# Kernel tuning notes

Measured on AMD Instinct MI355X. Metric: run time of the kernel, lower is better.

## Reference

```python
import jax, jax.numpy as jnp
import numpy as np

N, C, T, H, W = 8, 512, 8, 32, 32
CI = 256          # inter_channels = in_channels // 2
CA = 128          # audio feature dim (hard-coded nn.Linear(128, in_channels))
BN_EPS = 1e-5
LN_EPS = 1e-5


def setup_inputs() -> dict:
    key = jax.random.key(0)
    ks = jax.random.split(key, 8)
    s = 0.02
    f32 = jnp.float32
    return {
        "x": jax.random.normal(ks[0], (N, C, T, H, W), f32),
        "audio": jax.random.normal(ks[1], (N, T, CA), f32),
        "align_W": jax.random.normal(ks[2], (C, CA), f32) * s,
        "align_b": jnp.zeros((C,), f32),
        "Wg": jax.random.normal(ks[3], (CI, C), f32) * s,
        "bg": jnp.zeros((CI,), f32),
        "Wth": jax.random.normal(ks[4], (CI, C), f32) * s,
        "bth": jnp.zeros((CI,), f32),
        "Wph": jax.random.normal(ks[5], (CI, C), f32) * s,
        "bph": jnp.zeros((CI,), f32),
        "Wz": jax.random.normal(ks[6], (C, CI), f32) * s,
        "bz": jnp.zeros((C,), f32),
        "bn_gamma": jnp.ones((C,), f32),
        "bn_beta": jnp.zeros((C,), f32),
        "ln_gamma": jnp.ones((C,), f32),
        "ln_beta": jnp.zeros((C,), f32),
    }


def reference(x, audio, align_W, align_b, Wg, bg, Wth, bth, Wph, bph,
              Wz, bz, bn_gamma, bn_beta, ln_gamma, ln_beta):
    n, c, t, h, w = x.shape
    thw = t * h * w

    # align_channel: Linear(128, C) + ReLU on audio (N,T,128) -> (N,T,C)
    audio_temp = jax.nn.relu(jnp.einsum('ntk,ck->ntc', audio, align_W) + align_b)
    a = audio_temp.transpose(0, 2, 1)  # (N,C,T); broadcast over (H,W) kept implicit

    # 1x1x1 conv projections (== per-token linear maps)
    g_x = (jnp.einsum('oc,ncthw->nthwo', Wg, x) + bg).reshape(n, thw, CI)      # (N,THW,CI)
    theta_x = (jnp.einsum('oc,ncthw->nthwo', Wth, x) + bth).reshape(n, thw, CI)
    phi_a = jnp.einsum('oc,nct->not', Wph, a) + bph[None, :, None]             # (N,CI,T)

    # mode='dot' attention. phi(audio) is constant over (h,w): the full score
    # matrix f[n,s,(t,h,w)] equals f_small[n,s,t], so f@g factorizes exactly.
    f_small = jnp.einsum('nsi,nit->nst', theta_x, phi_a)   # (N,THW,T)
    f_div = f_small / thw                                  # f / N_tokens
    G = g_x.reshape(n, t, h * w, CI).sum(axis=2)           # (N,T,CI): sum of g over repeated hw
    y = jnp.einsum('nst,nto->nso', f_div, G)               # (N,THW,CI)
    y = y.transpose(0, 2, 1).reshape(n, CI, t, h, w)

    # W_z: 1x1x1 conv (CI->C) + BatchNorm3d (training-mode batch stats)
    W_y = jnp.einsum('oc,ncthw->nothw', Wz, y) + bz[None, :, None, None, None]
    mu = W_y.mean(axis=(0, 2, 3, 4), keepdims=True)
    var = W_y.var(axis=(0, 2, 3, 4), keepdims=True)
    W_y = (W_y - mu) * jax.lax.rsqrt(var + BN_EPS)
    W_y = W_y * bn_gamma[None, :, None, None, None] + bn_beta[None, :, None, None, None]

    # residual blend + LayerNorm over channel dim
    z = 0.5 * W_y + 0.5 * x
    zp = z.transpose(0, 2, 3, 4, 1)  # (N,T,H,W,C)
    mu2 = zp.mean(axis=-1, keepdims=True)
    var2 = zp.var(axis=-1, keepdims=True)
    zp = (zp - mu2) * jax.lax.rsqrt(var2 + LN_EPS) * ln_gamma + ln_beta
    z = zp.transpose(0, 4, 1, 2, 3)  # (N,C,T,H,W)
    return z, audio_temp
```

## Files before the change

### kernel.cpp

```cpp
#include <hip/hip_runtime.h>


typedef float __attribute__((ext_vector_type(2))) f32x2;

__device__ __forceinline__ float hsum4(float4 v) { return (v.x + v.y) + (v.z + v.w); }
__device__ __forceinline__ void fma4v(float4& a, float4 w, float4 x) {
    a.x = fmaf(w.x, x.x, a.x); a.y = fmaf(w.y, x.y, a.y);
    a.z = fmaf(w.z, x.z, a.z); a.w = fmaf(w.w, x.w, a.w);
}

__global__ __launch_bounds__(256) void k_stage1(
    const float* __restrict__ x, const float* __restrict__ audio,
    const float* __restrict__ alignW, const float* __restrict__ alignB,
    const float* __restrict__ Wph, const float* __restrict__ bph,
    const float* __restrict__ Wth, const float* __restrict__ bth,
    float* __restrict__ outA, float* __restrict__ constT, float* __restrict__ M,
    float* __restrict__ xsT)
{
    int b = blockIdx.x; int tid = threadIdx.x;
    __shared__ float al[128];
    __shared__ float atl[512];
    __shared__ float phil[256];
    __shared__ float red[256];
    if (b >= 64) {
        int row = (b - 64) * 4 + (tid >> 6);
        int lane = tid & 63;
        const float4* p = reinterpret_cast<const float4*>(x + (size_t)row * 1024);
        float s = 0.f;
        #pragma unroll
        for (int k = 0; k < 4; ++k) {
            float4 v = p[lane + 64 * k];
            s += v.x + v.y + v.z + v.w;
        }
        for (int off = 32; off > 0; off >>= 1) s += __shfl_down(s, off);
        if (lane == 0) {
            int n = row >> 12, c = (row >> 3) & 511, t = row & 7;
            xsT[((size_t)n * 8 + t) * 512 + c] = s;
        }
        return;
    }
    int n = b >> 3; int t = b & 7;
    if (tid < 32)
        reinterpret_cast<float4*>(al)[tid] =
            reinterpret_cast<const float4*>(audio + (n * 8 + t) * 128)[tid];
    __syncthreads();
    {
        const float4* W0 = reinterpret_cast<const float4*>(alignW + (size_t)tid * 128);
        const float4* W1 = reinterpret_cast<const float4*>(alignW + (size_t)(tid + 256) * 128);
        const float4* A4 = reinterpret_cast<const float4*>(al);
        float4 s00 = {0,0,0,0}, s01 = {0,0,0,0}, s10 = {0,0,0,0}, s11 = {0,0,0,0};
        #pragma unroll
        for (int k = 0; k < 32; k += 2) {
            float4 a0 = A4[k], a1 = A4[k + 1];
            fma4v(s00, W0[k], a0); fma4v(s01, W0[k + 1], a1);
            fma4v(s10, W1[k], a0); fma4v(s11, W1[k + 1], a1);
        }
        float v0 = fmaxf(alignB[tid] + hsum4(s00) + hsum4(s01), 0.f);
        float v1 = fmaxf(alignB[tid + 256] + hsum4(s10) + hsum4(s11), 0.f);
        atl[tid] = v0;       outA[(n * 8 + t) * 512 + tid] = v0;
        atl[tid + 256] = v1; outA[(n * 8 + t) * 512 + tid + 256] = v1;
    }
    __syncthreads();
    {
        const float4* Wp = reinterpret_cast<const float4*>(Wph + (size_t)tid * 512);
        const float4* At = reinterpret_cast<const float4*>(atl);
        float4 s0 = {0,0,0,0}, s1 = {0,0,0,0}, s2 = {0,0,0,0}, s3 = {0,0,0,0};
        #pragma unroll 4
        for (int k = 0; k < 128; k += 4) {
            fma4v(s0, Wp[k], At[k]);         fma4v(s1, Wp[k + 1], At[k + 1]);
            fma4v(s2, Wp[k + 2], At[k + 2]); fma4v(s3, Wp[k + 3], At[k + 3]);
        }
        float acc = bph[tid] + (hsum4(s0) + hsum4(s1)) + (hsum4(s2) + hsum4(s3));
        phil[tid] = acc;
        red[tid] = acc * bth[tid];
    }
    __syncthreads();
    for (int sr = 128; sr > 0; sr >>= 1) {
        if (tid < sr) red[tid] += red[tid + sr];
        __syncthreads();
    }
    if (tid == 0) constT[n * 8 + t] = red[0];
    {
        float a0 = 0, a1 = 0, a2 = 0, a3 = 0, c0 = 0, c1 = 0, c2 = 0, c3 = 0;
        #pragma unroll 2
        for (int i = 0; i < 256; i += 4) {
            float p0 = phil[i], p1 = phil[i + 1], p2 = phil[i + 2], p3 = phil[i + 3];
            const float* W = Wth + (size_t)i * 512 + tid;
            a0 = fmaf(W[0], p0, a0);    a1 = fmaf(W[512], p1, a1);
            a2 = fmaf(W[1024], p2, a2); a3 = fmaf(W[1536], p3, a3);
            const float* W2 = W + 256;
            c0 = fmaf(W2[0], p0, c0);    c1 = fmaf(W2[512], p1, c1);
            c2 = fmaf(W2[1024], p2, c2); c3 = fmaf(W2[1536], p3, c3);
        }
        M[n * 4096 + tid * 8 + t] = (a0 + a1) + (a2 + a3);
        M[n * 4096 + (tid + 256) * 8 + t] = (c0 + c1) + (c2 + c3);
    }
}

__global__ __launch_bounds__(512, 4) void k_stage2(
    const float* __restrict__ x, const float* __restrict__ M,
    const float* __restrict__ constT, const float* __restrict__ xsT,
    const float* __restrict__ Wg, const float* __restrict__ bg,
    const float* __restrict__ Wz,
    float* __restrict__ fs, float* __restrict__ Part, float* __restrict__ GW)
{
    int b = blockIdx.x; int tid = threadIdx.x;
    __shared__ float Ml[512][8];
    __shared__ float ldsT[8][8][130];
    __shared__ float partm[2][44];
    __shared__ float xsl[512];
    __shared__ float gl[256];
    if (b >= 512) {
        int b2 = b - 512; int n = b2 >> 3; int t = b2 & 7;
        xsl[tid] = xsT[((size_t)n * 8 + t) * 512 + tid];
        __syncthreads();
        if (tid < 256) {
            const float4* Wr = reinterpret_cast<const float4*>(Wg + (size_t)tid * 512);
            const float4* X4 = reinterpret_cast<const float4*>(xsl);
            float4 s0 = {0,0,0,0}, s1 = {0,0,0,0}, s2 = {0,0,0,0}, s3 = {0,0,0,0};
            #pragma unroll 4
            for (int k = 0; k < 128; k += 4) {
                fma4v(s0, Wr[k], X4[k]);         fma4v(s1, Wr[k + 1], X4[k + 1]);
                fma4v(s2, Wr[k + 2], X4[k + 2]); fma4v(s3, Wr[k + 3], X4[k + 3]);
            }
            gl[tid] = 1024.f * bg[tid] + (hsum4(s0) + hsum4(s1)) + (hsum4(s2) + hsum4(s3));
        }
        __syncthreads();
        {
            const float4* Wr = reinterpret_cast<const float4*>(Wz + (size_t)tid * 256);
            const float4* G4 = reinterpret_cast<const float4*>(gl);
            float4 s0 = {0,0,0,0}, s1 = {0,0,0,0}, s2 = {0,0,0,0}, s3 = {0,0,0,0};
            #pragma unroll 4
            for (int k = 0; k < 64; k += 4) {
                fma4v(s0, Wr[k], G4[k]);         fma4v(s1, Wr[k + 1], G4[k + 1]);
                fma4v(s2, Wr[k + 2], G4[k + 2]); fma4v(s3, Wr[k + 3], G4[k + 3]);
            }
            GW[((size_t)n * 8 + t) * 512 + tid] =
                (hsum4(s0) + hsum4(s1)) + (hsum4(s2) + hsum4(s3));
        }
        return;
    }
    int n = b >> 6; int s0i = (b & 63) << 7;
    int lane = tid & 63; int wv = tid >> 6;
    {
        const float4* src = reinterpret_cast<const float4*>(M + n * 4096);
        float4* dst = reinterpret_cast<float4*>(&Ml[0][0]);
        for (int i = tid; i < 1024; i += 512) dst[i] = src[i];
    }
    __syncthreads();
    const float* xb = x + (size_t)n * 4194304 + s0i + lane * 2;
    float2 p2[8];
    #pragma unroll
    for (int k = 0; k < 8; ++k) p2[k] = make_float2(0.f, 0.f);
    #pragma unroll 16
    for (int j = 0; j < 64; ++j) {
        int c = wv * 64 + j;
        float2 xv = *reinterpret_cast<const float2*>(xb + (size_t)c * 8192);
        float4 m0 = *reinterpret_cast<const float4*>(&Ml[c][0]);
        float4 m1 = *reinterpret_cast<const float4*>(&Ml[c][4]);
        p2[0].x = fmaf(xv.x, m0.x, p2[0].x); p2[0].y = fmaf(xv.y, m0.x, p2[0].y);
        p2[1].x = fmaf(xv.x, m0.y, p2[1].x); p2[1].y = fmaf(xv.y, m0.y, p2[1].y);
        p2[2].x = fmaf(xv.x, m0.z, p2[2].x); p2[2].y = fmaf(xv.y, m0.z, p2[2].y);
        p2[3].x = fmaf(xv.x, m0.w, p2[3].x); p2[3].y = fmaf(xv.y, m0.w, p2[3].y);
        p2[4].x = fmaf(xv.x, m1.x, p2[4].x); p2[4].y = fmaf(xv.y, m1.x, p2[4].y);
        p2[5].x = fmaf(xv.x, m1.y, p2[5].x); p2[5].y = fmaf(xv.y, m1.y, p2[5].y);
        p2[6].x = fmaf(xv.x, m1.z, p2[6].x); p2[6].y = fmaf(xv.y, m1.z, p2[6].y);
        p2[7].x = fmaf(xv.x, m1.w, p2[7].x); p2[7].y = fmaf(xv.y, m1.w, p2[7].y);
    }
    #pragma unroll
    for (int k = 0; k < 8; ++k)
        *reinterpret_cast<float2*>(&ldsT[wv][k][lane * 2]) = p2[k];
    __syncthreads();
    if (tid < 128) {
        int tok = tid; int wq = tid >> 6;
        const float* ct = constT + n * 8;
        float q[8];
        #pragma unroll
        for (int k = 0; k < 8; ++k) {
            float v = ct[k];
            #pragma unroll
            for (int g = 0; g < 8; ++g) v += ldsT[g][k][tok];
            q[k] = v;
        }
        float4* op = reinterpret_cast<float4*>(fs + ((size_t)n * 8192 + s0i + tok) * 8);
        op[0] = make_float4(q[0], q[1], q[2], q[3]);
        op[1] = make_float4(q[4], q[5], q[6], q[7]);
        float mom[44];
        {
            int idx = 8;
            for (int t1 = 0; t1 < 8; ++t1) {
                mom[t1] = q[t1];
                for (int t2 = t1; t2 < 8; ++t2) { mom[idx] = q[t1] * q[t2]; ++idx; }
            }
        }
        for (int k = 0; k < 44; ++k)
            for (int off = 32; off > 0; off >>= 1) mom[k] += __shfl_down(mom[k], off);
        if ((tid & 63) == 0)
            for (int k = 0; k < 44; ++k) partm[wq][k] = mom[k];
    }
    __syncthreads();
    if (tid < 44) Part[b * 44 + tid] = partm[0][tid] + partm[1][tid];
}

__global__ __launch_bounds__(512, 4) void k_final(
    const float* __restrict__ x, const float* __restrict__ fs,
    const float* __restrict__ Part, const float* __restrict__ GW,
    const float* __restrict__ bz, const float* __restrict__ bng, const float* __restrict__ bnb,
    const float* __restrict__ lng, const float* __restrict__ lnb,
    float* __restrict__ outZ)
{
    int b = blockIdx.x; int n = b >> 6; int s0 = (b & 63) << 7;
    int tid = threadIdx.x; int lane = tid & 63; int wv = tid >> 6;
    __shared__ float GWl[512][8];
    __shared__ float4 PKl[512];
    __shared__ float redS[2][8][130];
    __shared__ float Fl[64];
    __shared__ float S2l[512];
    if (tid < 352) {
        int n2 = tid / 44, k = tid % 44;
        float v = 0.f;
        for (int i = 0; i < 64; ++i) v += Part[(n2 * 64 + i) * 44 + k];
        if (k < 8) Fl[n2 * 8 + k] = v;
        else {
            int kk = k - 8; int t1 = 0;
            while (kk >= 8 - t1) { kk -= 8 - t1; ++t1; }
            int t2 = t1 + kk;
            S2l[n2 * 64 + t1 * 8 + t2] = v;
            S2l[n2 * 64 + t2 * 8 + t1] = v;
        }
    }
    __syncthreads();
    {
        int c = tid;
        const float r = 1.f / 8192.f;
        float meanu = 0.f, e2 = 0.f;
        float gmine[8];
        for (int n2 = 0; n2 < 8; ++n2) {
            float g[8];
            #pragma unroll
            for (int t = 0; t < 8; ++t) g[t] = GW[(n2 * 8 + t) * 512 + c];
            if (n2 == n) {
                #pragma unroll
                for (int t = 0; t < 8; ++t) gmine[t] = g[t];
            }
            #pragma unroll
            for (int t = 0; t < 8; ++t) meanu += Fl[n2 * 8 + t] * g[t];
            for (int t1 = 0; t1 < 8; ++t1)
                #pragma unroll
                for (int t2 = 0; t2 < 8; ++t2) e2 += S2l[n2 * 64 + t1 * 8 + t2] * g[t1] * g[t2];
        }
        const float invCnt = 1.f / 65536.f;
        meanu *= r * invCnt;
        e2 *= r * r * invCnt;
        float var = fmaxf(e2 - meanu * meanu, 0.f);
        float bzv = bz[c];
        float sc = bng[c] * rsqrtf(var + 1e-5f);
        float sh = bnb[c] - (meanu + bzv) * sc;
        float4 pk;
        pk.x = 0.5f * (bzv * sc + sh);
        pk.y = lng[c];
        pk.z = lnb[c];
        pk.w = 0.f;
        PKl[c] = pk;
        float scale = 0.5f * r * sc;
        #pragma unroll
        for (int t = 0; t < 8; ++t) GWl[c][t] = gmine[t] * scale;
    }
    __syncthreads();
    float4 fA0, fB0, fA1, fB1;
    {
        const float4* fp = reinterpret_cast<const float4*>(fs + ((size_t)n * 8192 + s0 + lane * 2) * 8);
        fA0 = fp[0]; fB0 = fp[1]; fA1 = fp[2]; fB1 = fp[3];
    }
    const size_t xbase = (size_t)n * 4194304 + s0 + lane * 2;
    float2 s1 = make_float2(0.f, 0.f), sq = make_float2(0.f, 0.f);
    #pragma unroll 16
    for (int j = 0; j < 64; ++j) {
        int c = wv * 64 + j;
        float2 xv = *reinterpret_cast<const float2*>(&x[xbase + (size_t)c * 8192]);
        float4 g0 = *reinterpret_cast<const float4*>(&GWl[c][0]);
        float4 g1 = *reinterpret_cast<const float4*>(&GWl[c][4]);
        float pk0 = PKl[c].x;
        float z0 = pk0 + 0.5f * xv.x
            + fA0.x * g0.x + fA0.y * g0.y + fA0.z * g0.z + fA0.w * g0.w
            + fB0.x * g1.x + fB0.y * g1.y + fB0.z * g1.z + fB0.w * g1.w;
        float z1 = pk0 + 0.5f * xv.y
            + fA1.x * g0.x + fA1.y * g0.y + fA1.z * g0.z + fA1.w * g0.w
            + fB1.x * g1.x + fB1.y * g1.y + fB1.z * g1.z + fB1.w * g1.w;
        s1.x += z0; sq.x += z0 * z0;
        s1.y += z1; sq.y += z1 * z1;
    }
    *reinterpret_cast<float2*>(&redS[0][wv][lane * 2]) = s1;
    *reinterpret_cast<float2*>(&redS[1][wv][lane * 2]) = sq;
    __syncthreads();
    float mean0, rstd0, mean1, rstd1;
    {
        int t0 = lane * 2, t1 = lane * 2 + 1;
        float a0 = 0.f, q0 = 0.f, a1 = 0.f, q1 = 0.f;
        #pragma unroll
        for (int g = 0; g < 8; ++g) {
            a0 += redS[0][g][t0]; q0 += redS[1][g][t0];
            a1 += redS[0][g][t1]; q1 += redS[1][g][t1];
        }
        mean0 = a0 * (1.f / 512.f);
        rstd0 = rsqrtf(fmaxf(q0 * (1.f / 512.f) - mean0 * mean0, 0.f) + 1e-5f);
        mean1 = a1 * (1.f / 512.f);
        rstd1 = rsqrtf(fmaxf(q1 * (1.f / 512.f) - mean1 * mean1, 0.f) + 1e-5f);
    }
    #pragma unroll 16
    for (int j = 0; j < 64; ++j) {
        int c = wv * 64 + j;
        float2 xv = *reinterpret_cast<const float2*>(&x[xbase + (size_t)c * 8192]);
        float4 g0 = *reinterpret_cast<const float4*>(&GWl[c][0]);
        float4 g1 = *reinterpret_cast<const float4*>(&GWl[c][4]);
        float4 pk = PKl[c];
        float z0 = pk.x + 0.5f * xv.x
            + fA0.x * g0.x + fA0.y * g0.y + fA0.z * g0.z + fA0.w * g0.w
            + fB0.x * g1.x + fB0.y * g1.y + fB0.z * g1.z + fB0.w * g1.w;
        float z1 = pk.x + 0.5f * xv.y
            + fA1.x * g0.x + fA1.y * g0.y + fA1.z * g0.z + fA1.w * g0.w
            + fB1.x * g1.x + fB1.y * g1.y + fB1.z * g1.z + fB1.w * g1.w;
        f32x2 o;
        o.x = (z0 - mean0) * rstd0 * pk.y + pk.z;
        o.y = (z1 - mean1) * rstd1 * pk.y + pk.z;
        __builtin_nontemporal_store(o, reinterpret_cast<f32x2*>(&outZ[xbase + (size_t)c * 8192]));
    }
}

extern "C" void kernel_launch(void* const* d_in, const int* in_sizes, int n_in,
                              void* d_out, int out_size, void* d_ws, size_t ws_size,
                              hipStream_t stream)
{
    const float* x      = (const float*)d_in[0];
    const float* audio  = (const float*)d_in[1];
    const float* alignW = (const float*)d_in[2];
    const float* alignB = (const float*)d_in[3];
    const float* Wg     = (const float*)d_in[4];
    const float* bg     = (const float*)d_in[5];
    const float* Wth    = (const float*)d_in[6];
    const float* bth    = (const float*)d_in[7];
    const float* Wph    = (const float*)d_in[8];
    const float* bph    = (const float*)d_in[9];
    const float* Wz     = (const float*)d_in[10];
    const float* bz     = (const float*)d_in[11];
    const float* bng    = (const float*)d_in[12];
    const float* bnb    = (const float*)d_in[13];
    const float* lng    = (const float*)d_in[14];
    const float* lnb    = (const float*)d_in[15];
    float* outZ = (float*)d_out;
    float* outA = outZ + 33554432;

    uintptr_t pa = ((uintptr_t)d_ws + 255) & ~(uintptr_t)255;
    float* w = (float*)pa;

    float* constT = w;
    float* M      = w + 64;
    float* XS     = w + 32832;
    float* GW     = w + 65600;
    float* Part   = w + 98368;
    float* fsm    = w + 120896;

    k_stage1<<<8256, 256, 0, stream>>>(x, audio, alignW, alignB, Wph, bph, Wth, bth,
                                       outA, constT, M, XS);
    k_stage2<<<576, 512, 0, stream>>>(x, M, constT, XS, Wg, bg, Wz, fsm, Part, GW);
    k_final<<<512, 512, 0, stream>>>(x, fsm, Part, GW, bz, bng, bnb, lng, lnb, outZ);
}
```

Before: 170.5 us.

## Fuse per-(n,c,t) spatial sums of x into stage2 pass, add small GW kernel

Removes the separate full pass over x in stage1 that computed per-(n,c,t) spatial sums. Those sums are now taken inside stage2's existing x stream via warp shuffles, written as per-block partials, and reduced by a new small kernel that also computes G and GW. This saves one full read of the 128MB input at the cost of an extra kernel launch and some shuffle work in the hot loop.

```diff
diff --git a/kernel.cpp b/kernel.cpp
--- a/kernel.cpp
+++ b/kernel.cpp
@@ -10,36 +10,18 @@
 }
 
 __global__ __launch_bounds__(256) void k_stage1(
-    const float* __restrict__ x, const float* __restrict__ audio,
+    const float* __restrict__ audio,
     const float* __restrict__ alignW, const float* __restrict__ alignB,
     const float* __restrict__ Wph, const float* __restrict__ bph,
     const float* __restrict__ Wth, const float* __restrict__ bth,
-    float* __restrict__ outA, float* __restrict__ constT, float* __restrict__ M,
-    float* __restrict__ xsT)
+    float* __restrict__ outA, float* __restrict__ constT, float* __restrict__ M)
 {
     int b = blockIdx.x; int tid = threadIdx.x;
+    int n = b >> 3; int t = b & 7;
     __shared__ float al[128];
     __shared__ float atl[512];
     __shared__ float phil[256];
     __shared__ float red[256];
-    if (b >= 64) {
-        int row = (b - 64) * 4 + (tid >> 6);
-        int lane = tid & 63;
-        const float4* p = reinterpret_cast<const float4*>(x + (size_t)row * 1024);
-        float s = 0.f;
-        #pragma unroll
-        for (int k = 0; k < 4; ++k) {
-            float4 v = p[lane + 64 * k];
-            s += v.x + v.y + v.z + v.w;
-        }
-        for (int off = 32; off > 0; off >>= 1) s += __shfl_down(s, off);
-        if (lane == 0) {
-            int n = row >> 12, c = (row >> 3) & 511, t = row & 7;
-            xsT[((size_t)n * 8 + t) * 512 + c] = s;
-        }
-        return;
-    }
-    int n = b >> 3; int t = b & 7;
     if (tid < 32)
         reinterpret_cast<float4*>(al)[tid] =
             reinterpret_cast<const float4*>(audio + (n * 8 + t) * 128)[tid];
@@ -99,49 +81,16 @@
 
 __global__ __launch_bounds__(512, 4) void k_stage2(
     const float* __restrict__ x, const float* __restrict__ M,
-    const float* __restrict__ constT, const float* __restrict__ xsT,
-    const float* __restrict__ Wg, const float* __restrict__ bg,
-    const float* __restrict__ Wz,
-    float* __restrict__ fs, float* __restrict__ Part, float* __restrict__ GW)
+    const float* __restrict__ constT, float* __restrict__ fs,
+    float* __restrict__ Part, float* __restrict__ Part2)
 {
     int b = blockIdx.x; int tid = threadIdx.x;
+    int n = b >> 6; int s0i = (b & 63) << 7;
+    int lane = tid & 63; int wv = tid >> 6;
     __shared__ float Ml[512][8];
     __shared__ float ldsT[8][8][130];
+    __shared__ float XsW[8][64];
     __shared__ float partm[2][44];
-    __shared__ float xsl[512];
-    __shared__ float gl[256];
-    if (b >= 512) {
-        int b2 = b - 512; int n = b2 >> 3; int t = b2 & 7;
-        xsl[tid] = xsT[((size_t)n * 8 + t) * 512 + tid];
-        __syncthreads();
-        if (tid < 256) {
-            const float4* Wr = reinterpret_cast<const float4*>(Wg + (size_t)tid * 512);
-            const float4* X4 = reinterpret_cast<const float4*>(xsl);
-            float4 s0 = {0,0,0,0}, s1 = {0,0,0,0}, s2 = {0,0,0,0}, s3 = {0,0,0,0};
-            #pragma unroll 4
-            for (int k = 0; k < 128; k += 4) {
-                fma4v(s0, Wr[k], X4[k]);         fma4v(s1, Wr[k + 1], X4[k + 1]);
-                fma4v(s2, Wr[k + 2], X4[k + 2]); fma4v(s3, Wr[k + 3], X4[k + 3]);
-            }
-            gl[tid] = 1024.f * bg[tid] + (hsum4(s0) + hsum4(s1)) + (hsum4(s2) + hsum4(s3));
-        }
-        __syncthreads();
-        {
-            const float4* Wr = reinterpret_cast<const float4*>(Wz + (size_t)tid * 256);
-            const float4* G4 = reinterpret_cast<const float4*>(gl);
-            float4 s0 = {0,0,0,0}, s1 = {0,0,0,0}, s2 = {0,0,0,0}, s3 = {0,0,0,0};
-            #pragma unroll 4
-            for (int k = 0; k < 64; k += 4) {
-                fma4v(s0, Wr[k], G4[k]);         fma4v(s1, Wr[k + 1], G4[k + 1]);
-                fma4v(s2, Wr[k + 2], G4[k + 2]); fma4v(s3, Wr[k + 3], G4[k + 3]);
-            }
-            GW[((size_t)n * 8 + t) * 512 + tid] =
-                (hsum4(s0) + hsum4(s1)) + (hsum4(s2) + hsum4(s3));
-        }
-        return;
-    }
-    int n = b >> 6; int s0i = (b & 63) << 7;
-    int lane = tid & 63; int wv = tid >> 6;
     {
         const float4* src = reinterpret_cast<const float4*>(M + n * 4096);
         float4* dst = reinterpret_cast<float4*>(&Ml[0][0]);
@@ -152,25 +101,42 @@
     float2 p2[8];
     #pragma unroll
     for (int k = 0; k < 8; ++k) p2[k] = make_float2(0.f, 0.f);
-    #pragma unroll 16
-    for (int j = 0; j < 64; ++j) {
-        int c = wv * 64 + j;
-        float2 xv = *reinterpret_cast<const float2*>(xb + (size_t)c * 8192);
-        float4 m0 = *reinterpret_cast<const float4*>(&Ml[c][0]);
-        float4 m1 = *reinterpret_cast<const float4*>(&Ml[c][4]);
-        p2[0].x = fmaf(xv.x, m0.x, p2[0].x); p2[0].y = fmaf(xv.y, m0.x, p2[0].y);
-        p2[1].x = fmaf(xv.x, m0.y, p2[1].x); p2[1].y = fmaf(xv.y, m0.y, p2[1].y);
-        p2[2].x = fmaf(xv.x, m0.z, p2[2].x); p2[2].y = fmaf(xv.y, m0.z, p2[2].y);
-        p2[3].x = fmaf(xv.x, m0.w, p2[3].x); p2[3].y = fmaf(xv.y, m0.w, p2[3].y);
-        p2[4].x = fmaf(xv.x, m1.x, p2[4].x); p2[4].y = fmaf(xv.y, m1.x, p2[4].y);
-        p2[5].x = fmaf(xv.x, m1.y, p2[5].x); p2[5].y = fmaf(xv.y, m1.y, p2[5].y);
-        p2[6].x = fmaf(xv.x, m1.z, p2[6].x); p2[6].y = fmaf(xv.y, m1.z, p2[6].y);
-        p2[7].x = fmaf(xv.x, m1.w, p2[7].x); p2[7].y = fmaf(xv.y, m1.w, p2[7].y);
+    #pragma unroll 4
+    for (int j4 = 0; j4 < 64; j4 += 4) {
+        float xs[4];
+        #pragma unroll
+        for (int u = 0; u < 4; ++u) {
+            int c = wv * 64 + j4 + u;
+            float2 xv = *reinterpret_cast<const float2*>(xb + (size_t)c * 8192);
+            float4 m0 = *reinterpret_cast<const float4*>(&Ml[c][0]);
+            float4 m1 = *reinterpret_cast<const float4*>(&Ml[c][4]);
+            p2[0].x = fmaf(xv.x, m0.x, p2[0].x); p2[0].y = fmaf(xv.y, m0.x, p2[0].y);
+            p2[1].x = fmaf(xv.x, m0.y, p2[1].x); p2[1].y = fmaf(xv.y, m0.y, p2[1].y);
+            p2[2].x = fmaf(xv.x, m0.z, p2[2].x); p2[2].y = fmaf(xv.y, m0.z, p2[2].y);
+            p2[3].x = fmaf(xv.x, m0.w, p2[3].x); p2[3].y = fmaf(xv.y, m0.w, p2[3].y);
+            p2[4].x = fmaf(xv.x, m1.x, p2[4].x); p2[4].y = fmaf(xv.y, m1.x, p2[4].y);
+            p2[5].x = fmaf(xv.x, m1.y, p2[5].x); p2[5].y = fmaf(xv.y, m1.y, p2[5].y);
+            p2[6].x = fmaf(xv.x, m1.z, p2[6].x); p2[6].y = fmaf(xv.y, m1.z, p2[6].y);
+            p2[7].x = fmaf(xv.x, m1.w, p2[7].x); p2[7].y = fmaf(xv.y, m1.w, p2[7].y);
+            xs[u] = xv.x + xv.y;
+        }
+        #pragma unroll
+        for (int off = 32; off > 0; off >>= 1) {
+            xs[0] += __shfl_down(xs[0], off);
+            xs[1] += __shfl_down(xs[1], off);
+            xs[2] += __shfl_down(xs[2], off);
+            xs[3] += __shfl_down(xs[3], off);
+        }
+        if (lane == 0) {
+            XsW[wv][j4]     = xs[0]; XsW[wv][j4 + 1] = xs[1];
+            XsW[wv][j4 + 2] = xs[2]; XsW[wv][j4 + 3] = xs[3];
+        }
     }
     #pragma unroll
     for (int k = 0; k < 8; ++k)
         *reinterpret_cast<float2*>(&ldsT[wv][k][lane * 2]) = p2[k];
     __syncthreads();
+    Part2[(size_t)b * 512 + tid] = XsW[tid >> 6][tid & 63];
     if (tid < 128) {
         int tok = tid; int wq = tid >> 6;
         const float* ct = constT + n * 8;
@@ -200,6 +166,48 @@
     }
     __syncthreads();
     if (tid < 44) Part[b * 44 + tid] = partm[0][tid] + partm[1][tid];
+}
+
+__global__ __launch_bounds__(512) void k_stage2b(
+    const float* __restrict__ Part2, const float* __restrict__ Wg,
+    const float* __restrict__ bg, const float* __restrict__ Wz,
+    float* __restrict__ GW)
+{
+    int b2 = blockIdx.x; int n = b2 >> 3; int t = b2 & 7; int tid = threadIdx.x;
+    __shared__ float xsl[512];
+    __shared__ float gl[256];
+    {
+        float v = 0.f;
+        #pragma unroll
+        for (int tb = 0; tb < 8; ++tb)
+            v += Part2[(size_t)(n * 64 + t * 8 + tb) * 512 + tid];
+        xsl[tid] = v;
+    }
+    __syncthreads();
+    if (tid < 256) {
+        const float4* Wr = reinterpret_cast<const float4*>(Wg + (size_t)tid * 512);
+        const float4* X4 = reinterpret_cast<const float4*>(xsl);
+        float4 s0 = {0,0,0,0}, s1 = {0,0,0,0}, s2 = {0,0,0,0}, s3 = {0,0,0,0};
+        #pragma unroll 4
+        for (int k = 0; k < 128; k += 4) {
+            fma4v(s0, Wr[k], X4[k]);         fma4v(s1, Wr[k + 1], X4[k + 1]);
+            fma4v(s2, Wr[k + 2], X4[k + 2]); fma4v(s3, Wr[k + 3], X4[k + 3]);
+        }
+        gl[tid] = 1024.f * bg[tid] + (hsum4(s0) + hsum4(s1)) + (hsum4(s2) + hsum4(s3));
+    }
+    __syncthreads();
+    {
+        const float4* Wr = reinterpret_cast<const float4*>(Wz + (size_t)tid * 256);
+        const float4* G4 = reinterpret_cast<const float4*>(gl);
+        float4 s0 = {0,0,0,0}, s1 = {0,0,0,0}, s2 = {0,0,0,0}, s3 = {0,0,0,0};
+        #pragma unroll 4
+        for (int k = 0; k < 64; k += 4) {
+            fma4v(s0, Wr[k], G4[k]);         fma4v(s1, Wr[k + 1], G4[k + 1]);
+            fma4v(s2, Wr[k + 2], G4[k + 2]); fma4v(s3, Wr[k + 3], G4[k + 3]);
+        }
+        GW[((size_t)n * 8 + t) * 512 + tid] =
+            (hsum4(s0) + hsum4(s1)) + (hsum4(s2) + hsum4(s3));
+    }
 }
 
 __global__ __launch_bounds__(512, 4) void k_final(
@@ -355,13 +363,14 @@
 
     float* constT = w;
     float* M      = w + 64;
-    float* XS     = w + 32832;
-    float* GW     = w + 65600;
-    float* Part   = w + 98368;
-    float* fsm    = w + 120896;
-
-    k_stage1<<<8256, 256, 0, stream>>>(x, audio, alignW, alignB, Wph, bph, Wth, bth,
-                                       outA, constT, M, XS);
-    k_stage2<<<576, 512, 0, stream>>>(x, M, constT, XS, Wg, bg, Wz, fsm, Part, GW);
+    float* GW     = w + 32832;
+    float* Part   = w + 65600;
+    float* Part2  = w + 88128;
+    float* fsm    = w + 350272;
+
+    k_stage1<<<64, 256, 0, stream>>>(audio, alignW, alignB, Wph, bph, Wth, bth,
+                                     outA, constT, M);
+    k_stage2<<<512, 512, 0, stream>>>(x, M, constT, fsm, Part, Part2);
+    k_stage2b<<<64, 512, 0, stream>>>(Part2, Wg, bg, Wz, GW);
     k_final<<<512, 512, 0, stream>>>(x, fsm, Part, GW, bz, bng, bnb, lng, lnb, outZ);
 }
```

Result: slower. 242.6 us (+42.3%).
